# Kernel tuning notes

Hardware: AMD Instinct MI355X
Metric: run time of the kernel (lower is better)

## Reference

```python
import jax, jax.numpy as jnp
import numpy as np

WINDOW_SIZE = 11
SIGMA = 1.5
CHANNELS = 3
WEIGHT = 0.1
DATA_RANGE = 1.0


def _gaussian_kernel(window_size, sigma, channels):
    coords = jnp.arange(window_size, dtype=jnp.float32) - window_size // 2
    g = jnp.exp(-coords ** 2 / (2.0 * sigma ** 2))
    g = g / g.sum()
    k2d = jnp.outer(g, g)  # (W, W)
    # OIHW depthwise kernel: (channels, 1, W, W)
    return jnp.tile(k2d[None, None, :, :], (channels, 1, 1, 1))


def _dwconv(x, window):
    pad = WINDOW_SIZE // 2
    return jax.lax.conv_general_dilated(
        x, window,
        window_strides=(1, 1),
        padding=[(pad, pad), (pad, pad)],
        dimension_numbers=("NCHW", "OIHW", "NCHW"),
        feature_group_count=CHANNELS,
    )


def setup_inputs() -> dict:
    key = jax.random.key(0)
    k1, k2 = jax.random.split(key)
    shape = (16, 3, 512, 512)
    pred = jax.random.uniform(k1, shape, dtype=jnp.float32)
    target = jax.random.uniform(k2, shape, dtype=jnp.float32)
    window = _gaussian_kernel(WINDOW_SIZE, SIGMA, CHANNELS)
    return {"pred": pred, "target": target, "window": window}


def reference(pred, target, window):
    C1 = (0.01 * DATA_RANGE) ** 2
    C2 = (0.03 * DATA_RANGE) ** 2
    mu1 = _dwconv(pred, window)
    mu2 = _dwconv(target, window)
    mu1_sq = mu1 * mu1
    mu2_sq = mu2 * mu2
    mu1_mu2 = mu1 * mu2
    sigma1_sq = _dwconv(pred * pred, window) - mu1_sq
    sigma2_sq = _dwconv(target * target, window) - mu2_sq
    sigma12 = _dwconv(pred * target, window) - mu1_mu2
    numerator = (2.0 * mu1_mu2 + C1) * (2.0 * sigma12 + C2)
    denominator = (mu1_sq + mu2_sq + C1) * (sigma1_sq + sigma2_sq + C2)
    ssim_val = jnp.mean(numerator / denominator)
    return WEIGHT * (1.0 - ssim_val)
```

## Files before the change

### kernel.cpp

```cpp
#include <hip/hip_runtime.h>

typedef _Float16 half8 __attribute__((ext_vector_type(8)));
typedef float f32x4 __attribute__((ext_vector_type(4)));

#define W 512
#define H 512
#define NPIX (16.0f*3.0f*512.0f*512.0f)
#define NACC 64
#define VSTR 88
#define VPLANE (64*VSTR)

__global__ __launch_bounds__(256) void ssim_main(const float* __restrict__ pred,
                                                 const float* __restrict__ targ,
                                                 const float* __restrict__ win,
                                                 float* __restrict__ acc) {
    const int tid  = threadIdx.x;
    const int lane = tid & 63;
    const int wv   = tid >> 6;
    const int lo   = lane & 15;
    const int hi   = lane >> 4;

    const int b = (blockIdx.x & 7) * 384 + (blockIdx.x >> 3);
    const int sx = b & 7, sy = (b >> 3) & 7, nc = b >> 6;
    const int x0 = sx * 64, y0 = sy * 64;
    const float* P = pred + (size_t)nc * (W * H);
    const float* T = targ + (size_t)nc * (W * H);

    __shared__ __align__(16) _Float16 VP[4 * VPLANE];
    __shared__ _Float16 gw[64];
    __shared__ float wsum[4];

    if (tid < 64) {
        const int d = tid - 18;
        float val = 0.f;
        if (d >= 0 && d <= 10)
            val = win[55 + d] * __builtin_amdgcn_rcpf(sqrtf(win[60]));
        gw[tid] = (_Float16)val;
    }
    __syncthreads();

    half8 Aw, Bw;
    #pragma unroll
    for (int j = 0; j < 8; ++j) {
        Aw[j] = gw[18 + hi * 8 + j - lo];
        Bw[j] = gw[15 + hi * 8 + j - lo];
    }

    const f32x4 zero4 = {0.f, 0.f, 0.f, 0.f};

    #pragma unroll
    for (int tc5 = 0; tc5 < 5; ++tc5) {
        const int col   = x0 - 8 + 16 * tc5 + lo;
        const int rbase = y0 - 5 + 16 * wv + hi * 8;
        float pf[8], tf[8];
        const bool fastpos = (y0 - 5 + 16 * wv >= 0) && (y0 - 5 + 16 * wv + 31 < H)
                          && (x0 - 8 + 16 * tc5 >= 0) && (x0 - 8 + 16 * tc5 + 15 < W);
        if (fastpos) {
            const float* Pp = P + (size_t)rbase * W + col;
            const float* Tp = T + (size_t)rbase * W + col;
            #pragma unroll
            for (int j = 0; j < 8; ++j) { pf[j] = Pp[j * W]; tf[j] = Tp[j * W]; }
        } else {
            const bool cok = (unsigned)col < W;
            const int  ccl = cok ? col : 0;
            #pragma unroll
            for (int j = 0; j < 8; ++j) {
                const int  r   = rbase + j;
                const bool rok = (unsigned)r < H;
                const int  rcl = rok ? r : 0;
                const float pv = P[(size_t)rcl * W + ccl];
                const float tv = T[(size_t)rcl * W + ccl];
                pf[j] = (rok && cok) ? pv : 0.f;
                tf[j] = (rok && cok) ? tv : 0.f;
            }
        }
        half8 pa, ta, qa, xa;
        #pragma unroll
        for (int j = 0; j < 8; ++j) {
            pa[j] = (_Float16)pf[j];
            ta[j] = (_Float16)tf[j];
            qa[j] = (_Float16)fmaf(tf[j], tf[j], pf[j] * pf[j]);
            xa[j] = (_Float16)(pf[j] * tf[j]);
        }
        const f32x4 d0 = __builtin_amdgcn_mfma_f32_16x16x32_f16(Aw, pa, zero4, 0, 0, 0);
        const f32x4 d1 = __builtin_amdgcn_mfma_f32_16x16x32_f16(Aw, ta, zero4, 0, 0, 0);
        const f32x4 d2 = __builtin_amdgcn_mfma_f32_16x16x32_f16(Aw, qa, zero4, 0, 0, 0);
        const f32x4 d3 = __builtin_amdgcn_mfma_f32_16x16x32_f16(Aw, xa, zero4, 0, 0, 0);
        const int vcol = 16 * tc5 + lo;
        #pragma unroll
        for (int reg = 0; reg < 4; ++reg) {
            const int base = (16 * wv + hi * 4 + reg) * VSTR + vcol;
            VP[0 * VPLANE + base] = (_Float16)d0[reg];
            VP[1 * VPLANE + base] = (_Float16)d1[reg];
            VP[2 * VPLANE + base] = (_Float16)d2[reg];
            VP[3 * VPLANE + base] = (_Float16)d3[reg];
        }
    }
    __syncthreads();

    const float C1 = 1e-4f, C2 = 9e-4f;
    float sum = 0.f;
    #pragma unroll
    for (int tc2 = 0; tc2 < 4; ++tc2) {
        const int ai = (16 * wv + lo) * VSTR + 16 * tc2 + hi * 8;
        const half8 a0 = *(const half8*)&VP[0 * VPLANE + ai];
        const half8 a1 = *(const half8*)&VP[1 * VPLANE + ai];
        const half8 a2 = *(const half8*)&VP[2 * VPLANE + ai];
        const half8 a3 = *(const half8*)&VP[3 * VPLANE + ai];
        const f32x4 m1 = __builtin_amdgcn_mfma_f32_16x16x32_f16(a0, Bw, zero4, 0, 0, 0);
        const f32x4 m2 = __builtin_amdgcn_mfma_f32_16x16x32_f16(a1, Bw, zero4, 0, 0, 0);
        const f32x4 qq = __builtin_amdgcn_mfma_f32_16x16x32_f16(a2, Bw, zero4, 0, 0, 0);
        const f32x4 pt = __builtin_amdgcn_mfma_f32_16x16x32_f16(a3, Bw, zero4, 0, 0, 0);
        #pragma unroll
        for (int r = 0; r < 4; ++r) {
            const float mu1 = m1[r], mu2 = m2[r];
            const float ms  = fmaf(mu1, mu1, mu2 * mu2);
            const float m12 = mu1 * mu2;
            const float s12 = pt[r] - m12;
            const float ssm = qq[r] - ms;
            const float num = fmaf(2.f, m12, C1) * fmaf(2.f, s12, C2);
            const float den = (ms + C1) * (ssm + C2);
            sum += num * __builtin_amdgcn_rcpf(den);
        }
    }

    #pragma unroll
    for (int off = 32; off > 0; off >>= 1) sum += __shfl_down(sum, off, 64);
    if (lane == 0) wsum[wv] = sum;
    __syncthreads();
    if (tid == 0)
        atomicAdd(&acc[blockIdx.x & (NACC - 1)], wsum[0] + wsum[1] + wsum[2] + wsum[3]);
}

__global__ void ssim_final(const float* __restrict__ acc, float* __restrict__ out) {
    float s = 0.f;
    #pragma unroll
    for (int i = 0; i < NACC; ++i) s += acc[i];
    out[0] = 0.1f * (1.0f - s / NPIX);
}

extern "C" void kernel_launch(void* const* d_in, const int* in_sizes, int n_in,
                              void* d_out, int out_size, void* d_ws, size_t ws_size,
                              hipStream_t stream) {
    const float* pred = (const float*)d_in[0];
    const float* targ = (const float*)d_in[1];
    const float* win  = (const float*)d_in[2];
    float* out = (float*)d_out;
    float* acc = (float*)d_ws;

    hipMemsetAsync(acc, 0, NACC * sizeof(float), stream);
    ssim_main<<<3072, 256, 0, stream>>>(pred, targ, win, acc);
    ssim_final<<<1, 1, 0, stream>>>(acc, out);
}
```

Baseline: 46.93 us.

## Swap separable conv order: horizontal pass first with row-vector loads, 64x32 tiles

```diff
diff --git a/kernel.cpp b/kernel.cpp
--- a/kernel.cpp
+++ b/kernel.cpp
@@ -1,14 +1,15 @@
 #include <hip/hip_runtime.h>
 
 typedef _Float16 half8 __attribute__((ext_vector_type(8)));
+typedef _Float16 half4 __attribute__((ext_vector_type(4)));
 typedef float f32x4 __attribute__((ext_vector_type(4)));
 
 #define W 512
 #define H 512
 #define NPIX (16.0f*3.0f*512.0f*512.0f)
 #define NACC 64
-#define VSTR 88
-#define VPLANE (64*VSTR)
+#define TSTR 56
+#define TPL (64*TSTR)
 
 __global__ __launch_bounds__(256) void ssim_main(const float* __restrict__ pred,
                                                  const float* __restrict__ targ,
@@ -20,13 +21,13 @@
     const int lo   = lane & 15;
     const int hi   = lane >> 4;
 
-    const int b = (blockIdx.x & 7) * 384 + (blockIdx.x >> 3);
-    const int sx = b & 7, sy = (b >> 3) & 7, nc = b >> 6;
-    const int x0 = sx * 64, y0 = sy * 64;
+    const int b = (blockIdx.x & 7) * 768 + (blockIdx.x >> 3);
+    const int sx = b & 7, sy = (b >> 3) & 15, nc = b >> 7;
+    const int x0 = sx * 64, y0 = sy * 32;
     const float* P = pred + (size_t)nc * (W * H);
     const float* T = targ + (size_t)nc * (W * H);
 
-    __shared__ __align__(16) _Float16 VP[4 * VPLANE];
+    __shared__ __align__(16) _Float16 TP[4 * TPL];
     __shared__ _Float16 gw[64];
     __shared__ float wsum[4];
 
@@ -39,39 +40,41 @@
     }
     __syncthreads();
 
-    half8 Aw, Bw;
+    half8 Bh, Bv;
     #pragma unroll
     for (int j = 0; j < 8; ++j) {
-        Aw[j] = gw[18 + hi * 8 + j - lo];
-        Bw[j] = gw[15 + hi * 8 + j - lo];
+        Bh[j] = gw[15 + hi * 8 + j - lo];
+        Bv[j] = gw[18 + hi * 8 + j - lo];
     }
 
     const f32x4 zero4 = {0.f, 0.f, 0.f, 0.f};
+    const int  cbase   = x0 + wv * 16 - 8 + hi * 8;
+    const bool colsafe = (x0 + wv * 16 - 8 >= 0) && (x0 + wv * 16 + 23 < W);
 
     #pragma unroll
-    for (int tc5 = 0; tc5 < 5; ++tc5) {
-        const int col   = x0 - 8 + 16 * tc5 + lo;
-        const int rbase = y0 - 5 + 16 * wv + hi * 8;
+    for (int rt = 0; rt < 3; ++rt) {
+        const int rowbase = y0 - 5 + rt * 16;
+        const int row = rowbase + lo;
         float pf[8], tf[8];
-        const bool fastpos = (y0 - 5 + 16 * wv >= 0) && (y0 - 5 + 16 * wv + 31 < H)
-                          && (x0 - 8 + 16 * tc5 >= 0) && (x0 - 8 + 16 * tc5 + 15 < W);
-        if (fastpos) {
-            const float* Pp = P + (size_t)rbase * W + col;
-            const float* Tp = T + (size_t)rbase * W + col;
-            #pragma unroll
-            for (int j = 0; j < 8; ++j) { pf[j] = Pp[j * W]; tf[j] = Tp[j * W]; }
+        if (colsafe && rowbase >= 0 && rowbase + 15 < H) {
+            const float* Pp = P + (size_t)row * W + cbase;
+            const float* Tp = T + (size_t)row * W + cbase;
+            *(float4*)&pf[0] = *(const float4*)Pp;
+            *(float4*)&pf[4] = *(const float4*)(Pp + 4);
+            *(float4*)&tf[0] = *(const float4*)Tp;
+            *(float4*)&tf[4] = *(const float4*)(Tp + 4);
         } else {
-            const bool cok = (unsigned)col < W;
-            const int  ccl = cok ? col : 0;
+            const bool rok = (unsigned)row < H;
+            const int  rid = rok ? row : 0;
             #pragma unroll
             for (int j = 0; j < 8; ++j) {
-                const int  r   = rbase + j;
-                const bool rok = (unsigned)r < H;
-                const int  rcl = rok ? r : 0;
-                const float pv = P[(size_t)rcl * W + ccl];
-                const float tv = T[(size_t)rcl * W + ccl];
-                pf[j] = (rok && cok) ? pv : 0.f;
-                tf[j] = (rok && cok) ? tv : 0.f;
+                const int  c  = cbase + j;
+                const int  ci = ((unsigned)c < W) ? c : 0;
+                const bool ok = rok && ((unsigned)c < W);
+                const float pv = P[(size_t)rid * W + ci];
+                const float tv = T[(size_t)rid * W + ci];
+                pf[j] = ok ? pv : 0.f;
+                tf[j] = ok ? tv : 0.f;
             }
         }
         half8 pa, ta, qa, xa;
@@ -82,18 +85,22 @@
             qa[j] = (_Float16)fmaf(tf[j], tf[j], pf[j] * pf[j]);
             xa[j] = (_Float16)(pf[j] * tf[j]);
         }
-        const f32x4 d0 = __builtin_amdgcn_mfma_f32_16x16x32_f16(Aw, pa, zero4, 0, 0, 0);
-        const f32x4 d1 = __builtin_amdgcn_mfma_f32_16x16x32_f16(Aw, ta, zero4, 0, 0, 0);
-        const f32x4 d2 = __builtin_amdgcn_mfma_f32_16x16x32_f16(Aw, qa, zero4, 0, 0, 0);
-        const f32x4 d3 = __builtin_amdgcn_mfma_f32_16x16x32_f16(Aw, xa, zero4, 0, 0, 0);
-        const int vcol = 16 * tc5 + lo;
-        #pragma unroll
-        for (int reg = 0; reg < 4; ++reg) {
-            const int base = (16 * wv + hi * 4 + reg) * VSTR + vcol;
-            VP[0 * VPLANE + base] = (_Float16)d0[reg];
-            VP[1 * VPLANE + base] = (_Float16)d1[reg];
-            VP[2 * VPLANE + base] = (_Float16)d2[reg];
-            VP[3 * VPLANE + base] = (_Float16)d3[reg];
+        f32x4 d0 = __builtin_amdgcn_mfma_f32_16x16x32_f16(pa, Bh, zero4, 0, 0, 0);
+        f32x4 d1 = __builtin_amdgcn_mfma_f32_16x16x32_f16(ta, Bh, zero4, 0, 0, 0);
+        f32x4 d2 = __builtin_amdgcn_mfma_f32_16x16x32_f16(qa, Bh, zero4, 0, 0, 0);
+        f32x4 d3 = __builtin_amdgcn_mfma_f32_16x16x32_f16(xa, Bh, zero4, 0, 0, 0);
+        const int tbase = (wv * 16 + lo) * TSTR + rt * 16 + hi * 4;
+        {
+            half4 h0, h1, h2, h3;
+            #pragma unroll
+            for (int r = 0; r < 4; ++r) {
+                h0[r] = (_Float16)d0[r]; h1[r] = (_Float16)d1[r];
+                h2[r] = (_Float16)d2[r]; h3[r] = (_Float16)d3[r];
+            }
+            *(half4*)&TP[0 * TPL + tbase] = h0;
+            *(half4*)&TP[1 * TPL + tbase] = h1;
+            *(half4*)&TP[2 * TPL + tbase] = h2;
+            *(half4*)&TP[3 * TPL + tbase] = h3;
         }
     }
     __syncthreads();
@@ -101,16 +108,16 @@
     const float C1 = 1e-4f, C2 = 9e-4f;
     float sum = 0.f;
     #pragma unroll
-    for (int tc2 = 0; tc2 < 4; ++tc2) {
-        const int ai = (16 * wv + lo) * VSTR + 16 * tc2 + hi * 8;
-        const half8 a0 = *(const half8*)&VP[0 * VPLANE + ai];
-        const half8 a1 = *(const half8*)&VP[1 * VPLANE + ai];
-        const half8 a2 = *(const half8*)&VP[2 * VPLANE + ai];
-        const half8 a3 = *(const half8*)&VP[3 * VPLANE + ai];
-        const f32x4 m1 = __builtin_amdgcn_mfma_f32_16x16x32_f16(a0, Bw, zero4, 0, 0, 0);
-        const f32x4 m2 = __builtin_amdgcn_mfma_f32_16x16x32_f16(a1, Bw, zero4, 0, 0, 0);
-        const f32x4 qq = __builtin_amdgcn_mfma_f32_16x16x32_f16(a2, Bw, zero4, 0, 0, 0);
-        const f32x4 pt = __builtin_amdgcn_mfma_f32_16x16x32_f16(a3, Bw, zero4, 0, 0, 0);
+    for (int rtv = 0; rtv < 2; ++rtv) {
+        const int abase = (wv * 16 + lo) * TSTR + rtv * 16 + hi * 8;
+        const half8 a0 = *(const half8*)&TP[0 * TPL + abase];
+        const half8 a1 = *(const half8*)&TP[1 * TPL + abase];
+        const half8 a2 = *(const half8*)&TP[2 * TPL + abase];
+        const half8 a3 = *(const half8*)&TP[3 * TPL + abase];
+        const f32x4 m1 = __builtin_amdgcn_mfma_f32_16x16x32_f16(a0, Bv, zero4, 0, 0, 0);
+        const f32x4 m2 = __builtin_amdgcn_mfma_f32_16x16x32_f16(a1, Bv, zero4, 0, 0, 0);
+        const f32x4 qq = __builtin_amdgcn_mfma_f32_16x16x32_f16(a2, Bv, zero4, 0, 0, 0);
+        const f32x4 pt = __builtin_amdgcn_mfma_f32_16x16x32_f16(a3, Bv, zero4, 0, 0, 0);
         #pragma unroll
         for (int r = 0; r < 4; ++r) {
             const float mu1 = m1[r], mu2 = m2[r];
@@ -149,6 +156,6 @@
     float* acc = (float*)d_ws;
 
     hipMemsetAsync(acc, 0, NACC * sizeof(float), stream);
-    ssim_main<<<3072, 256, 0, stream>>>(pred, targ, win, acc);
+    ssim_main<<<6144, 256, 0, stream>>>(pred, targ, win, acc);
     ssim_final<<<1, 1, 0, stream>>>(acc, out);
 }
```

Result: slower. 63.38 us (+35.1%).

## Make SSIM blocks persistent with double-buffered staging and software-pipelined tile loads

Applied to the files above, without the earlier changes.

```diff
diff --git a/kernel.cpp b/kernel.cpp
--- a/kernel.cpp
+++ b/kernel.cpp
@@ -1,14 +1,25 @@
 #include <hip/hip_runtime.h>
 
 typedef _Float16 half8 __attribute__((ext_vector_type(8)));
+typedef _Float16 half4 __attribute__((ext_vector_type(4)));
 typedef float f32x4 __attribute__((ext_vector_type(4)));
 
 #define W 512
 #define H 512
 #define NPIX (16.0f*3.0f*512.0f*512.0f)
 #define NACC 64
-#define VSTR 88
-#define VPLANE (64*VSTR)
+#define SROWS 78
+#define SSTR 52
+#define AH 4056
+#define ARRB 8112
+#define TPSTR 80
+#define TPL 2560
+#define NT 8
+
+#define LGKM0()  asm volatile("s_waitcnt lgkmcnt(0)" ::: "memory")
+#define VMCNT0() asm volatile("s_waitcnt vmcnt(0)" ::: "memory")
+#define BAR()    { asm volatile("" ::: "memory"); __builtin_amdgcn_s_barrier(); asm volatile("" ::: "memory"); }
+#define MFMA(A,B) __builtin_amdgcn_mfma_f32_16x16x32_f16((A),(B),zero4,0,0,0)
 
 __global__ __launch_bounds__(256) void ssim_main(const float* __restrict__ pred,
                                                  const float* __restrict__ targ,
@@ -20,13 +31,9 @@
     const int lo   = lane & 15;
     const int hi   = lane >> 4;
 
-    const int b = (blockIdx.x & 7) * 384 + (blockIdx.x >> 3);
-    const int sx = b & 7, sy = (b >> 3) & 7, nc = b >> 6;
-    const int x0 = sx * 64, y0 = sy * 64;
-    const float* P = pred + (size_t)nc * (W * H);
-    const float* T = targ + (size_t)nc * (W * H);
-
-    __shared__ __align__(16) _Float16 VP[4 * VPLANE];
+    __shared__ _Float16 stageA[2 * AH];
+    __shared__ _Float16 stageB[2 * AH];
+    __shared__ _Float16 TP[4 * TPL];
     __shared__ _Float16 gw[64];
     __shared__ float wsum[4];
 
@@ -37,91 +44,168 @@
             val = win[55 + d] * __builtin_amdgcn_rcpf(sqrtf(win[60]));
         gw[tid] = (_Float16)val;
     }
+    {
+        const half4 z4 = {(_Float16)0.f, (_Float16)0.f, (_Float16)0.f, (_Float16)0.f};
+        #pragma unroll
+        for (int i = 0; i < 10; ++i)
+            *(half4*)&TP[4 * (i * 256 + tid)] = z4;
+    }
     __syncthreads();
 
-    half8 Aw, Bw;
-    #pragma unroll
-    for (int j = 0; j < 8; ++j) {
-        Aw[j] = gw[18 + hi * 8 + j - lo];
+    half8 Bw;
+    #pragma unroll
+    for (int j = 0; j < 8; ++j)
         Bw[j] = gw[15 + hi * 8 + j - lo];
+
+    int pr[8], pc[8], wo[8];
+    #pragma unroll
+    for (int s = 0; s < 8; ++s) {
+        const int id  = s * 256 + tid;
+        const bool ok = id < 1872;
+        const int arr = (id >= 936) ? 1 : 0;
+        const int cid = id - 936 * arr;
+        const int r   = (cid * 5462) >> 16;
+        const int cc  = cid - r * 12;
+        pr[s] = ok ? r : (1 << 20);
+        pc[s] = cc * 4 - 8;
+        wo[s] = ok ? (arr * ARRB + r * 104 + cc * 8) : -1;
     }
 
     const f32x4 zero4 = {0.f, 0.f, 0.f, 0.f};
-
-    #pragma unroll
-    for (int tc5 = 0; tc5 < 5; ++tc5) {
-        const int col   = x0 - 8 + 16 * tc5 + lo;
-        const int rbase = y0 - 5 + 16 * wv + hi * 8;
-        float pf[8], tf[8];
-        const bool fastpos = (y0 - 5 + 16 * wv >= 0) && (y0 - 5 + 16 * wv + 31 < H)
-                          && (x0 - 8 + 16 * tc5 >= 0) && (x0 - 8 + 16 * tc5 + 15 < W);
-        if (fastpos) {
-            const float* Pp = P + (size_t)rbase * W + col;
-            const float* Tp = T + (size_t)rbase * W + col;
-            #pragma unroll
-            for (int j = 0; j < 8; ++j) { pf[j] = Pp[j * W]; tf[j] = Tp[j * W]; }
-        } else {
-            const bool cok = (unsigned)col < W;
-            const int  ccl = cok ? col : 0;
-            #pragma unroll
-            for (int j = 0; j < 8; ++j) {
-                const int  r   = rbase + j;
-                const bool rok = (unsigned)r < H;
-                const int  rcl = rok ? r : 0;
-                const float pv = P[(size_t)rcl * W + ccl];
-                const float tv = T[(size_t)rcl * W + ccl];
-                pf[j] = (rok && cok) ? pv : 0.f;
-                tf[j] = (rok && cok) ? tv : 0.f;
-            }
+    const float C1 = 1e-4f, C2 = 9e-4f;
+    f32x4 pre[8];
+    float sum = 0.f;
+
+    const int bsw = (blockIdx.x & 7) * 96 + (blockIdx.x >> 3);
+    const int t0  = bsw * NT;
+
+#define LOADREGS(tidx)                                                       \
+    {                                                                        \
+        const int nc = (tidx) >> 7, rem = (tidx) & 127;                      \
+        const int y0 = (rem >> 4) * 64, x0 = (rem & 15) * 32;                \
+        const float* Pb = pred + (size_t)nc * (W * H);                       \
+        const float* Tb = targ + (size_t)nc * (W * H);                       \
+        _Pragma("unroll")                                                    \
+        for (int s = 0; s < 8; ++s) {                                        \
+            const int gy = y0 - 8 + pr[s];                                   \
+            const int gx = x0 + pc[s];                                       \
+            const bool ok = ((unsigned)gy < H) && ((unsigned)gx < W);        \
+            const float* bp = (wo[s] >= ARRB) ? Tb : Pb;                     \
+            f32x4 v = zero4;                                                 \
+            if (ok) v = *(const f32x4*)(bp + (size_t)gy * W + gx);           \
+            pre[s] = v;                                                      \
+        }                                                                    \
+        __builtin_amdgcn_sched_barrier(0);          \
+    }
+
+#define WRITES(BUF)                                                          \
+    {                                                                        \
+        _Pragma("unroll")                                                    \
+        for (int s = 0; s < 8; ++s) {                                        \
+            if (wo[s] >= 0) {                                                \
+                half4 hv;                                                    \
+                hv[0] = (_Float16)pre[s][0]; hv[1] = (_Float16)pre[s][1];    \
+                hv[2] = (_Float16)pre[s][2]; hv[3] = (_Float16)pre[s][3];    \
+                *(half4*)((char*)(BUF) + wo[s]) = hv;                        \
+            }                                                                \
+        }                                                                    \
+    }
+
+#define HPASS(BUF)                                                           \
+    {                                                                        \
+        _Pragma("unroll")                                                    \
+        for (int it = 0; it < 3; ++it) {                                     \
+            const int t = wv + it * 4;                                       \
+            if (t < 10) {                                                    \
+                const int rt = t >> 1, ct = t & 1;                           \
+                const int hb = (rt * 16 + lo) * SSTR + ct * 16 + hi * 8;     \
+                const half4 pA = *(const half4*)(BUF + hb);                  \
+                const half4 pB = *(const half4*)(BUF + hb + 4);              \
+                const half4 tA = *(const half4*)(BUF + AH + hb);             \
+                const half4 tB = *(const half4*)(BUF + AH + hb + 4);         \
+                const half8 pa = __builtin_shufflevector(pA, pB, 0,1,2,3,4,5,6,7); \
+                const half8 ta = __builtin_shufflevector(tA, tB, 0,1,2,3,4,5,6,7); \
+                const half8 qa = pa * pa + ta * ta;                          \
+                const half8 xa = pa * ta;                                    \
+                const f32x4 d0 = MFMA(pa, Bw);                               \
+                const f32x4 d1 = MFMA(ta, Bw);                               \
+                const f32x4 d2 = MFMA(qa, Bw);                               \
+                const f32x4 d3 = MFMA(xa, Bw);                               \
+                const int tb = (ct * 16 + lo) * TPSTR + rt * 16 + hi * 4;    \
+                if (rt == 4 && hi == 3) {           \
+                    TP[0 * TPL + tb] = (_Float16)d0[0];                      \
+                    TP[1 * TPL + tb] = (_Float16)d1[0];                      \
+                    TP[2 * TPL + tb] = (_Float16)d2[0];                      \
+                    TP[3 * TPL + tb] = (_Float16)d3[0];                      \
+                } else {                                                     \
+                    half4 h0, h1, h2, h3;                                    \
+                    _Pragma("unroll")                                        \
+                    for (int r = 0; r < 4; ++r) {                            \
+                        h0[r] = (_Float16)d0[r]; h1[r] = (_Float16)d1[r];    \
+                        h2[r] = (_Float16)d2[r]; h3[r] = (_Float16)d3[r];    \
+                    }                                                        \
+                    *(half4*)&TP[0 * TPL + tb] = h0;                         \
+                    *(half4*)&TP[1 * TPL + tb] = h1;                         \
+                    *(half4*)&TP[2 * TPL + tb] = h2;                         \
+                    *(half4*)&TP[3 * TPL + tb] = h3;                         \
+                }                                                            \
+            }                                                                \
+        }                                                                    \
+    }
+
+#define VPASS()                                                              \
+    {                                                                        \
+        _Pragma("unroll")                                                    \
+        for (int iv = 0; iv < 2; ++iv) {                                     \
+            const int v = wv + iv * 4;                                       \
+            const int rtv = v >> 1, ct = v & 1;                              \
+            const int ah = (ct * 16 + lo) * TPSTR + rtv * 16 + hi * 8;       \
+            const half8 a0 = *(const half8*)&TP[0 * TPL + ah];               \
+            const half8 a1 = *(const half8*)&TP[1 * TPL + ah];               \
+            const half8 a2 = *(const half8*)&TP[2 * TPL + ah];               \
+            const half8 a3 = *(const half8*)&TP[3 * TPL + ah];               \
+            const f32x4 m1 = MFMA(a0, Bw);                                   \
+            const f32x4 m2 = MFMA(a1, Bw);                                   \
+            const f32x4 qq = MFMA(a2, Bw);                                   \
+            const f32x4 pt = MFMA(a3, Bw);                                   \
+            _Pragma("unroll")                                                \
+            for (int r = 0; r < 4; ++r) {                                    \
+                const float mu1 = m1[r], mu2 = m2[r];                        \
+                const float ms  = fmaf(mu1, mu1, mu2 * mu2);                 \
+                const float m12 = mu1 * mu2;                                 \
+                const float s12 = pt[r] - m12;                               \
+                const float ssm = qq[r] - ms;                                \
+                const float num = fmaf(2.f, m12, C1) * fmaf(2.f, s12, C2);   \
+                const float den = (ms + C1) * (ssm + C2);                    \
+                sum += num * __builtin_amdgcn_rcpf(den);                     \
+            }                                                                \
+        }                                                                    \
+    }
+
+    LOADREGS(t0);
+    VMCNT0();
+    WRITES(stageA);
+    LGKM0(); BAR();
+
+    #pragma unroll 1
+    for (int i = 0; i < NT; i += 2) {
+        LOADREGS(t0 + i + 1);
+        HPASS(stageA);
+        LGKM0(); BAR();
+        VPASS();
+        VMCNT0();
+        WRITES(stageB);
+        LGKM0(); BAR();
+
+        if (i + 2 < NT) LOADREGS(t0 + i + 2);
+        HPASS(stageB);
+        LGKM0(); BAR();
+        VPASS();
+        if (i + 2 < NT) {
+            VMCNT0();
+            WRITES(stageA);
         }
-        half8 pa, ta, qa, xa;
-        #pragma unroll
-        for (int j = 0; j < 8; ++j) {
-            pa[j] = (_Float16)pf[j];
-            ta[j] = (_Float16)tf[j];
-            qa[j] = (_Float16)fmaf(tf[j], tf[j], pf[j] * pf[j]);
-            xa[j] = (_Float16)(pf[j] * tf[j]);
-        }
-        const f32x4 d0 = __builtin_amdgcn_mfma_f32_16x16x32_f16(Aw, pa, zero4, 0, 0, 0);
-        const f32x4 d1 = __builtin_amdgcn_mfma_f32_16x16x32_f16(Aw, ta, zero4, 0, 0, 0);
-        const f32x4 d2 = __builtin_amdgcn_mfma_f32_16x16x32_f16(Aw, qa, zero4, 0, 0, 0);
-        const f32x4 d3 = __builtin_amdgcn_mfma_f32_16x16x32_f16(Aw, xa, zero4, 0, 0, 0);
-        const int vcol = 16 * tc5 + lo;
-        #pragma unroll
-        for (int reg = 0; reg < 4; ++reg) {
-            const int base = (16 * wv + hi * 4 + reg) * VSTR + vcol;
-            VP[0 * VPLANE + base] = (_Float16)d0[reg];
-            VP[1 * VPLANE + base] = (_Float16)d1[reg];
-            VP[2 * VPLANE + base] = (_Float16)d2[reg];
-            VP[3 * VPLANE + base] = (_Float16)d3[reg];
-        }
-    }
-    __syncthreads();
-
-    const float C1 = 1e-4f, C2 = 9e-4f;
-    float sum = 0.f;
-    #pragma unroll
-    for (int tc2 = 0; tc2 < 4; ++tc2) {
-        const int ai = (16 * wv + lo) * VSTR + 16 * tc2 + hi * 8;
-        const half8 a0 = *(const half8*)&VP[0 * VPLANE + ai];
-        const half8 a1 = *(const half8*)&VP[1 * VPLANE + ai];
-        const half8 a2 = *(const half8*)&VP[2 * VPLANE + ai];
-        const half8 a3 = *(const half8*)&VP[3 * VPLANE + ai];
-        const f32x4 m1 = __builtin_amdgcn_mfma_f32_16x16x32_f16(a0, Bw, zero4, 0, 0, 0);
-        const f32x4 m2 = __builtin_amdgcn_mfma_f32_16x16x32_f16(a1, Bw, zero4, 0, 0, 0);
-        const f32x4 qq = __builtin_amdgcn_mfma_f32_16x16x32_f16(a2, Bw, zero4, 0, 0, 0);
-        const f32x4 pt = __builtin_amdgcn_mfma_f32_16x16x32_f16(a3, Bw, zero4, 0, 0, 0);
-        #pragma unroll
-        for (int r = 0; r < 4; ++r) {
-            const float mu1 = m1[r], mu2 = m2[r];
-            const float ms  = fmaf(mu1, mu1, mu2 * mu2);
-            const float m12 = mu1 * mu2;
-            const float s12 = pt[r] - m12;
-            const float ssm = qq[r] - ms;
-            const float num = fmaf(2.f, m12, C1) * fmaf(2.f, s12, C2);
-            const float den = (ms + C1) * (ssm + C2);
-            sum += num * __builtin_amdgcn_rcpf(den);
-        }
+        LGKM0(); BAR();
     }
 
     #pragma unroll
@@ -129,7 +213,11 @@
     if (lane == 0) wsum[wv] = sum;
     __syncthreads();
     if (tid == 0)
-        atomicAdd(&acc[blockIdx.x & (NACC - 1)], wsum[0] + wsum[1] + wsum[2] + wsum[3]);
+        atomicAdd(&acc[bsw & (NACC - 1)], wsum[0] + wsum[1] + wsum[2] + wsum[3]);
+#undef LOADREGS
+#undef WRITES
+#undef HPASS
+#undef VPASS
 }
 
 __global__ void ssim_final(const float* __restrict__ acc, float* __restrict__ out) {
@@ -149,6 +237,6 @@
     float* acc = (float*)d_ws;
 
     hipMemsetAsync(acc, 0, NACC * sizeof(float), stream);
-    ssim_main<<<3072, 256, 0, stream>>>(pred, targ, win, acc);
+    ssim_main<<<768, 256, 0, stream>>>(pred, targ, win, acc);
     ssim_final<<<1, 1, 0, stream>>>(acc, out);
 }
```

Measured after the change: 49.48 us. 5.4% more time.
